# Kernel tuning notes

Measured on AMD Instinct MI355X. Metric: run time of the kernel, lower is better.

## Reference

```python
import jax, jax.numpy as jnp
import numpy as np

N, E, D = 100000, 1600000, 128
BN_EPS = 1e-5


def setup_inputs() -> dict:
    key = jax.random.key(0)
    k0, k1, k2 = jax.random.split(key, 3)
    x = jax.random.normal(k0, (N, D), dtype=jnp.float32)
    edge_index = jax.random.randint(k1, (2, E), 0, N, dtype=jnp.int32)
    # GCNConv weight (glorot-ish scale) and bias
    W = jax.random.normal(k2, (D, D), dtype=jnp.float32) * (1.0 / np.sqrt(D))
    b = jnp.zeros((D,), dtype=jnp.float32)
    # BatchNorm1d affine params
    gamma = jnp.ones((D,), dtype=jnp.float32)
    beta = jnp.zeros((D,), dtype=jnp.float32)
    # PReLU single shared slope (torch default init 0.25)
    a_prelu = jnp.asarray(0.25, dtype=jnp.float32)
    return {"x": x, "W": W, "b": b, "gamma": gamma, "beta": beta,
            "a_prelu": a_prelu, "edge_index": edge_index}


def reference(x, W, b, gamma, beta, a_prelu, edge_index):
    n = x.shape[0]
    loops = jnp.arange(n, dtype=edge_index.dtype)
    src = jnp.concatenate([edge_index[0], loops])  # [E+N]
    dst = jnp.concatenate([edge_index[1], loops])  # [E+N]

    # GCN symmetric normalization with self-loops: deg counts incoming edges
    deg = jax.ops.segment_sum(jnp.ones_like(dst, dtype=x.dtype), dst, num_segments=n)
    dinv = jax.lax.rsqrt(deg)  # deg >= 1 thanks to self-loops
    enorm = dinv[src] * dinv[dst]  # [E+N]

    xw = x @ W                                        # [N, D] transform first
    msg = xw[src] * enorm[:, None]                    # gather + scale
    out = jax.ops.segment_sum(msg, dst, num_segments=n) + b  # scatter-add

    # BatchNorm1d over nodes (training-mode batch statistics, biased var)
    mean = jnp.mean(out, axis=0)
    var = jnp.mean(jnp.square(out - mean), axis=0)
    out = (out - mean) * jax.lax.rsqrt(var + BN_EPS) * gamma + beta

    # PReLU (single shared slope); dropout is identity in eval mode
    out = jnp.where(out > 0, out, a_prelu * out)

    # identity residual (in_dim == out_dim)
    return out + x
```

## Files before the change

kernel.cpp:

```cpp
#include <hip/hip_runtime.h>

#define DIM 128
#define BSH 8
#define BUCK 256
#define CAP2 6144
#define BINCH 2048
#define MAXB 1024
#define FPT 12

typedef __attribute__((ext_vector_type(8))) short bf16x8;
typedef __attribute__((ext_vector_type(4))) float f32x4;
union U8 { uint4 u; bf16x8 b; };

static __device__ __forceinline__ unsigned f2bf_bits(float f) {
  unsigned u = __float_as_uint(f);
  return (u + 0x7fffu + ((u >> 16) & 1u)) >> 16;
}
static __device__ __forceinline__ unsigned packbf(float a, float b) {
  return (f2bf_bits(a) & 0xffffu) | (f2bf_bits(b) << 16);
}
static __device__ __forceinline__ float bfu_lo(unsigned pk) { return __uint_as_float(pk << 16); }
static __device__ __forceinline__ float bfu_hi(unsigned pk) { return __uint_as_float(pk & 0xffff0000u); }

static __device__ __forceinline__ int eread(const int* __restrict__ e, long long idx, int fl64) {
  return fl64 ? e[idx * 2] : e[idx];
}

__global__ __launch_bounds__(256) void k_prep(const int* __restrict__ eidx, int E,
                                              int* __restrict__ bcnt,
                                              unsigned* __restrict__ tmp2, int nbuck,
                                              const float* __restrict__ W,
                                              unsigned* __restrict__ wbt,
                                              int NBB) {
  __shared__ int hist[MAXB];
  __shared__ int lcur[MAXB];
  __shared__ int sfl;
  int bid = blockIdx.x;
  int tid = threadIdx.x;

  if (bid < NBB) {
    if (tid < 64) {
      int w = eidx[tid * 2 + 1];
      unsigned long long m = __ballot(w == 0);
      if (tid == 0) sfl = (__popcll(m) >= 48) ? 1 : 0;
    }
    for (int i = tid; i < nbuck; i += 256) hist[i] = 0;
    __syncthreads();
    int fl = sfl;
    long long ebase = (long long)bid * BINCH;
    unsigned pk[BINCH / 256];
    int bb[BINCH / 256];
#pragma unroll
    for (int it = 0; it < BINCH / 256; ++it) {
      long long e = ebase + it * 256 + tid;
      bb[it] = -1;
      if (e < E) {
        int s = eread(eidx, e, fl);
        int d = eread(eidx, (long long)E + e, fl);
        bb[it] = d >> BSH;
        pk[it] = ((unsigned)s << BSH) | (unsigned)(d & (BUCK - 1));
        atomicAdd(&hist[bb[it]], 1);
      }
    }
    __syncthreads();
    for (int b = tid; b < nbuck; b += 256) {
      int h = hist[b];
      lcur[b] = h ? atomicAdd(&bcnt[b], h) : 0;
    }
    __syncthreads();
#pragma unroll
    for (int it = 0; it < BINCH / 256; ++it) {
      if (bb[it] >= 0) {
        int sl = atomicAdd(&lcur[bb[it]], 1);
        if (sl < CAP2) tmp2[(unsigned)bb[it] * CAP2 + sl] = pk[it];
      }
    }
  } else {
    int w = (bid - NBB) * 256 + tid;
    int c = w >> 6, kk = w & 63;
    float lo = W[(unsigned)(2 * kk) * DIM + c];
    float hi = W[(unsigned)(2 * kk + 1) * DIM + c];
    wbt[(unsigned)c * 64 + kk] = packbf(lo, hi);
  }
}

__global__ __launch_bounds__(512) void k_histsort(const int* __restrict__ bcnt,
                                                  unsigned* __restrict__ tmp2,
                                                  int* __restrict__ ofs2,
                                                  int* __restrict__ deg,
                                                  const float* __restrict__ x,
                                                  unsigned* __restrict__ xb, int n) {
  __shared__ unsigned srt[CAP2];
  __shared__ int hist[BUCK];
  __shared__ int sc2[BUCK];
  __shared__ int lcur[BUCK];
  __shared__ float dls[BUCK];
  int b = blockIdx.x, tid = threadIdx.x;
  int cnt = bcnt[b];
  if (cnt > CAP2) cnt = CAP2;
  unsigned base = (unsigned)b * CAP2;
  if (tid < BUCK) hist[tid] = 0;
  __syncthreads();
  unsigned r[FPT];
#pragma unroll
  for (int u = 0; u < FPT; ++u) {
    int j = u * 512 + tid;
    r[u] = 0xffffffffu;
    if (j < cnt) {
      r[u] = tmp2[base + j];
      atomicAdd(&hist[r[u] & (BUCK - 1)], 1);
    }
  }
  __syncthreads();
  if (tid < 64) {
    int h0 = hist[tid * 4], h1 = hist[tid * 4 + 1];
    int h2 = hist[tid * 4 + 2], h3 = hist[tid * 4 + 3];
    int s = h0 + h1 + h2 + h3;
    int pre = s;
#pragma unroll
    for (int d = 1; d < 64; d <<= 1) {
      int t = __shfl_up(pre, d);
      if (tid >= d) pre += t;
    }
    pre -= s;
    int e0 = pre, e1 = pre + h0, e2 = e1 + h1, e3 = e2 + h2;
    sc2[tid * 4] = e0;     lcur[tid * 4] = e0;
    sc2[tid * 4 + 1] = e1; lcur[tid * 4 + 1] = e1;
    sc2[tid * 4 + 2] = e2; lcur[tid * 4 + 2] = e2;
    sc2[tid * 4 + 3] = e3; lcur[tid * 4 + 3] = e3;
  }
  __syncthreads();
#pragma unroll
  for (int u = 0; u < FPT; ++u) {
    if (r[u] != 0xffffffffu) {
      int sl = atomicAdd(&lcur[r[u] & (BUCK - 1)], 1);
      srt[sl] = r[u];
    }
  }
  if (tid < BUCK) dls[tid] = rsqrtf((float)(hist[tid] + 1));
  __syncthreads();
#pragma unroll
  for (int u = 0; u < FPT; ++u) {
    int j = u * 512 + tid;
    if (j < cnt) tmp2[base + j] = srt[j];
  }
  if (tid < BUCK) {
    int node = b * BUCK + tid;
    if (node < n) {
      ofs2[node] = (int)base + sc2[tid];
      deg[node] = hist[tid];
    }
  }
  int nb0 = b * BUCK;
#pragma unroll
  for (int it = 0; it < 32; ++it) {
    int idx = it * 512 + tid;
    int ln = idx >> 6, p = idx & 63;
    int node = nb0 + ln;
    if (node < n) {
      float di = dls[ln];
      float2 v = *(const float2*)(x + (size_t)node * DIM + p * 2);
      xb[(unsigned)node * 64 + p] = packbf(v.x * di, v.y * di);
    }
  }
}

__global__ __launch_bounds__(256) void k_agg(const unsigned* __restrict__ tmp2,
                                             const unsigned* __restrict__ xb,
                                             const int* __restrict__ ofs2,
                                             const int* __restrict__ deg,
                                             unsigned* __restrict__ agg, int n) {
  int wid = blockIdx.x * 4 + (threadIdx.x >> 6);
  int lane = threadIdx.x & 63;
  if (wid >= n) return;
  int dg = __builtin_amdgcn_readfirstlane(deg[wid]);
  float di = rsqrtf((float)(dg + 1));
  unsigned xp = xb[(unsigned)wid * 64 + lane];
  float ax = bfu_lo(xp), ay = bfu_hi(xp);
  int e = __builtin_amdgcn_readfirstlane(ofs2[wid]);
  int e1 = e + dg;
  for (; e + 16 <= e1; e += 16) {
    unsigned s[16];
#pragma unroll
    for (int u = 0; u < 16; ++u) s[u] = tmp2[(unsigned)(e + u)] >> BSH;
    unsigned v[16];
#pragma unroll
    for (int u = 0; u < 16; ++u) v[u] = xb[s[u] * 64 + lane];
#pragma unroll
    for (int u = 0; u < 16; ++u) { ax += bfu_lo(v[u]); ay += bfu_hi(v[u]); }
  }
  for (; e + 4 <= e1; e += 4) {
    unsigned s0 = tmp2[(unsigned)e] >> BSH, s1 = tmp2[(unsigned)e + 1] >> BSH;
    unsigned s2 = tmp2[(unsigned)e + 2] >> BSH, s3 = tmp2[(unsigned)e + 3] >> BSH;
    unsigned v0 = xb[s0 * 64 + lane], v1 = xb[s1 * 64 + lane];
    unsigned v2 = xb[s2 * 64 + lane], v3 = xb[s3 * 64 + lane];
    ax += bfu_lo(v0); ay += bfu_hi(v0);
    ax += bfu_lo(v1); ay += bfu_hi(v1);
    ax += bfu_lo(v2); ay += bfu_hi(v2);
    ax += bfu_lo(v3); ay += bfu_hi(v3);
  }
  for (; e < e1; ++e) {
    unsigned vv = xb[(tmp2[(unsigned)e] >> BSH) * 64 + lane];
    ax += bfu_lo(vv); ay += bfu_hi(vv);
  }
  agg[(unsigned)wid * 64 + lane] = packbf(ax * di, ay * di);
}

__global__ __launch_bounds__(256) void k_gemm(
    const unsigned* __restrict__ agg, const unsigned* __restrict__ wbt,
    const float* __restrict__ bias, unsigned* __restrict__ preb,
    float* __restrict__ part, int n) {
  __shared__ unsigned SM[64 * 68 + 128 * 68];
  unsigned* As2 = SM;
  unsigned* WsT = SM + 64 * 68;
  int tid = threadIdx.x;
  int base = blockIdx.x * 64;

#pragma unroll
  for (int it = 0; it < 32; ++it) {
    int idx = it * 256 + tid;
    int c = idx >> 6, kk = idx & 63;
    WsT[c * 68 + kk] = wbt[idx];
  }
#pragma unroll
  for (int it = 0; it < 16; ++it) {
    int idx = it * 256 + tid;
    int rl = idx >> 6, c2 = idx & 63;
    int g = base + rl; if (g >= n) g = n - 1;
    As2[rl * 68 + c2] = agg[(unsigned)g * 64 + c2];
  }
  __syncthreads();

  int w = tid >> 6, l = tid & 63;
  int lg = l >> 4, lr = l & 15;
  f32x4 acc[8];
#pragma unroll
  for (int nt = 0; nt < 8; ++nt) acc[nt] = (f32x4){0.f, 0.f, 0.f, 0.f};

#pragma unroll
  for (int kt = 0; kt < 4; ++kt) {
    U8 bfr;
    bfr.u = *(const uint4*)&As2[(w * 16 + lr) * 68 + kt * 16 + lg * 4];
#pragma unroll
    for (int nt = 0; nt < 8; ++nt) {
      U8 afr;
      afr.u = *(const uint4*)&WsT[(nt * 16 + lr) * 68 + kt * 16 + lg * 4];
      acc[nt] = __builtin_amdgcn_mfma_f32_16x16x32_bf16(afr.b, bfr.b, acc[nt], 0, 0, 0);
    }
  }
  __syncthreads();

  float* Cf = (float*)SM;
#pragma unroll
  for (int nt = 0; nt < 8; ++nt) {
    *(f32x4*)&Cf[(w * 16 + lr) * 132 + nt * 16 + lg * 4] = acc[nt];
  }
  __syncthreads();

  float* bn = Cf + 64 * 132;
  int c2 = tid & 63, g4 = tid >> 6;
  float b0 = bias[2 * c2], b1 = bias[2 * c2 + 1];
  float cs0 = 0.f, cs1 = 0.f, cq0 = 0.f, cq1 = 0.f;
#pragma unroll
  for (int it = 0; it < 16; ++it) {
    int m = it * 4 + g4;
    int gg = base + m;
    float2 vv = *(const float2*)&Cf[m * 132 + 2 * c2];
    float v0 = vv.x + b0, v1 = vv.y + b1;
    if (gg < n) {
      preb[(unsigned)gg * 64 + c2] = packbf(v0, v1);
      cs0 += v0; cq0 += v0 * v0;
      cs1 += v1; cq1 += v1 * v1;
    }
  }
  bn[g4 * 256 + 2 * c2] = cs0;
  bn[g4 * 256 + 2 * c2 + 1] = cs1;
  bn[g4 * 256 + 128 + 2 * c2] = cq0;
  bn[g4 * 256 + 128 + 2 * c2 + 1] = cq1;
  __syncthreads();
  part[(size_t)blockIdx.x * 256 + tid] = bn[tid] + bn[256 + tid] + bn[512 + tid] + bn[768 + tid];
}

__global__ __launch_bounds__(256) void k_redbn(const float* __restrict__ part, int nb,
                                               const float* __restrict__ gma,
                                               const float* __restrict__ bta,
                                               float* __restrict__ sc_,
                                               float* __restrict__ sh_, float invn) {
  __shared__ float r1[256], r2[256];
  int c = blockIdx.x, t = threadIdx.x;
  float s = 0.f, q = 0.f;
  for (int i = t; i < nb; i += 256) {
    s += part[(size_t)i * 256 + c];
    q += part[(size_t)i * 256 + 128 + c];
  }
  r1[t] = s; r2[t] = q;
  __syncthreads();
  for (int k = 128; k > 0; k >>= 1) {
    if (t < k) { r1[t] += r1[t + k]; r2[t] += r2[t + k]; }
    __syncthreads();
  }
  if (t == 0) {
    float mean = r1[0] * invn;
    float var = r2[0] * invn - mean * mean;
    float inv = rsqrtf(var + 1e-5f);
    float g = gma[c] * inv;
    sc_[c] = g;
    sh_[c] = bta[c] - mean * g;
  }
}

__global__ __launch_bounds__(256) void k_final(const unsigned* __restrict__ preb,
                                               const float* __restrict__ x,
                                               const float* __restrict__ sc,
                                               const float* __restrict__ sh,
                                               const float* __restrict__ apre,
                                               float* __restrict__ out, int n) {
  int t = blockIdx.x * 256 + threadIdx.x;
  int i = t >> 6, p = t & 63;
  if (i >= n) return;
  float a = apre[0];
  int c = p * 2;
  unsigned pk = preb[(unsigned)i * 64 + p];
  float t0 = bfu_lo(pk) * sc[c] + sh[c];
  float t1 = bfu_hi(pk) * sc[c + 1] + sh[c + 1];
  t0 = t0 > 0.f ? t0 : a * t0;
  t1 = t1 > 0.f ? t1 : a * t1;
  float2 xv = *(const float2*)(x + (size_t)i * DIM + c);
  t0 += xv.x;
  t1 += xv.y;
  *(float2*)(out + (size_t)i * DIM + c) = make_float2(t0, t1);
}

extern "C" void kernel_launch(void* const* d_in, const int* in_sizes, int n_in,
                              void* d_out, int out_size, void* d_ws, size_t ws_size,
                              hipStream_t stream) {
  (void)n_in; (void)out_size; (void)ws_size;
  const float* x    = (const float*)d_in[0];
  const float* W    = (const float*)d_in[1];
  const float* b    = (const float*)d_in[2];
  const float* gma  = (const float*)d_in[3];
  const float* bta  = (const float*)d_in[4];
  const float* apre = (const float*)d_in[5];
  const int* eidx   = (const int*)d_in[6];
  float* out        = (float*)d_out;

  const int N = in_sizes[0] / DIM;
  const int E = in_sizes[6] / 2;
  const int NB = (N + 63) / 64;
  const int NBUCK = (N + BUCK - 1) >> BSH;
  const int NBB = (E + BINCH - 1) / BINCH;
  const int NWT = 32;

  char* wsb = (char*)d_ws;
  size_t off_b = 0;
  auto take = [&](size_t bytes) -> void* {
    void* p = wsb + off_b;
    off_b += (bytes + 255) & ~(size_t)255;
    return p;
  };
  int*      bcnt  = (int*)     take((size_t)NBUCK * 4);
  int*      ofs2  = (int*)     take((size_t)N * 4);
  int*      deg   = (int*)     take((size_t)N * 4);
  unsigned* wbt   = (unsigned*)take((size_t)DIM * 64 * 4);
  unsigned* tmp2  = (unsigned*)take((size_t)NBUCK * CAP2 * 4);
  unsigned* xb    = (unsigned*)take((size_t)N * 64 * 4);
  unsigned* agg   = (unsigned*)take((size_t)N * 64 * 4);
  float*    part  = (float*)   take((size_t)NB * 256 * 4);
  float*    sc    = (float*)   take(DIM * 4);
  float*    sh    = (float*)   take(DIM * 4);
  unsigned* preb  = agg;

  hipMemsetAsync(bcnt, 0, (size_t)NBUCK * 4, stream);

  k_prep     <<<NBB + NWT, 256, 0, stream>>>(eidx, E, bcnt, tmp2, NBUCK, W, wbt, NBB);
  k_histsort <<<NBUCK, 512, 0, stream>>>(bcnt, tmp2, ofs2, deg, x, xb, N);
  k_agg      <<<(N + 3) / 4, 256, 0, stream>>>(tmp2, xb, ofs2, deg, agg, N);
  k_gemm     <<<NB, 256, 0, stream>>>(agg, wbt, b, preb, part, N);
  k_redbn    <<<DIM, 256, 0, stream>>>(part, NB, gma, bta, sc, sh, 1.0f / (float)N);
  k_final    <<<(N * 64 + 255) / 256, 256, 0, stream>>>(preb, x, sc, sh, apre, out, N);
}
```

Baseline: 271.8 us.

## Fuse neighbor aggregation into GEMM kernel with dynamic row scheduling in shared memory

Result: faster. 256.6 us (-5.6%).

```diff
diff --git a/kernel.cpp b/kernel.cpp
--- a/kernel.cpp
+++ b/kernel.cpp
@@ -153,107 +153,107 @@
   }
   int nb0 = b * BUCK;
 #pragma unroll
-  for (int it = 0; it < 32; ++it) {
+  for (int it = 0; it < 16; ++it) {
     int idx = it * 512 + tid;
-    int ln = idx >> 6, p = idx & 63;
+    int ln = idx >> 5, p = idx & 31;
     int node = nb0 + ln;
     if (node < n) {
       float di = dls[ln];
-      float2 v = *(const float2*)(x + (size_t)node * DIM + p * 2);
-      xb[(unsigned)node * 64 + p] = packbf(v.x * di, v.y * di);
-    }
-  }
-}
-
-__global__ __launch_bounds__(256) void k_agg(const unsigned* __restrict__ tmp2,
-                                             const unsigned* __restrict__ xb,
-                                             const int* __restrict__ ofs2,
-                                             const int* __restrict__ deg,
-                                             unsigned* __restrict__ agg, int n) {
-  int wid = blockIdx.x * 4 + (threadIdx.x >> 6);
-  int lane = threadIdx.x & 63;
-  if (wid >= n) return;
-  int dg = __builtin_amdgcn_readfirstlane(deg[wid]);
-  float di = rsqrtf((float)(dg + 1));
-  unsigned xp = xb[(unsigned)wid * 64 + lane];
-  float ax = bfu_lo(xp), ay = bfu_hi(xp);
-  int e = __builtin_amdgcn_readfirstlane(ofs2[wid]);
-  int e1 = e + dg;
-  for (; e + 16 <= e1; e += 16) {
-    unsigned s[16];
-#pragma unroll
-    for (int u = 0; u < 16; ++u) s[u] = tmp2[(unsigned)(e + u)] >> BSH;
-    unsigned v[16];
-#pragma unroll
-    for (int u = 0; u < 16; ++u) v[u] = xb[s[u] * 64 + lane];
-#pragma unroll
-    for (int u = 0; u < 16; ++u) { ax += bfu_lo(v[u]); ay += bfu_hi(v[u]); }
-  }
-  for (; e + 4 <= e1; e += 4) {
-    unsigned s0 = tmp2[(unsigned)e] >> BSH, s1 = tmp2[(unsigned)e + 1] >> BSH;
-    unsigned s2 = tmp2[(unsigned)e + 2] >> BSH, s3 = tmp2[(unsigned)e + 3] >> BSH;
-    unsigned v0 = xb[s0 * 64 + lane], v1 = xb[s1 * 64 + lane];
-    unsigned v2 = xb[s2 * 64 + lane], v3 = xb[s3 * 64 + lane];
-    ax += bfu_lo(v0); ay += bfu_hi(v0);
-    ax += bfu_lo(v1); ay += bfu_hi(v1);
-    ax += bfu_lo(v2); ay += bfu_hi(v2);
-    ax += bfu_lo(v3); ay += bfu_hi(v3);
-  }
-  for (; e < e1; ++e) {
-    unsigned vv = xb[(tmp2[(unsigned)e] >> BSH) * 64 + lane];
-    ax += bfu_lo(vv); ay += bfu_hi(vv);
-  }
-  agg[(unsigned)wid * 64 + lane] = packbf(ax * di, ay * di);
-}
-
-__global__ __launch_bounds__(256) void k_gemm(
-    const unsigned* __restrict__ agg, const unsigned* __restrict__ wbt,
-    const float* __restrict__ bias, unsigned* __restrict__ preb,
-    float* __restrict__ part, int n) {
+      float4 v = *(const float4*)(x + (size_t)node * DIM + p * 4);
+      uint2 o;
+      o.x = packbf(v.x * di, v.y * di);
+      o.y = packbf(v.z * di, v.w * di);
+      *(uint2*)&xb[(unsigned)node * 64 + p * 2] = o;
+    }
+  }
+}
+
+__global__ __launch_bounds__(1024) void k_agemm(
+    const unsigned* __restrict__ tmp2, const unsigned* __restrict__ xb,
+    const int* __restrict__ ofs2, const int* __restrict__ deg,
+    const unsigned* __restrict__ wbt, const float* __restrict__ bias,
+    unsigned* __restrict__ preb, float* __restrict__ part, int n) {
   __shared__ unsigned SM[64 * 68 + 128 * 68];
   unsigned* As2 = SM;
   unsigned* WsT = SM + 64 * 68;
+  __shared__ int nextn;
   int tid = threadIdx.x;
   int base = blockIdx.x * 64;
-
-#pragma unroll
-  for (int it = 0; it < 32; ++it) {
-    int idx = it * 256 + tid;
-    int c = idx >> 6, kk = idx & 63;
-    WsT[c * 68 + kk] = wbt[idx];
-  }
-#pragma unroll
-  for (int it = 0; it < 16; ++it) {
-    int idx = it * 256 + tid;
-    int rl = idx >> 6, c2 = idx & 63;
-    int g = base + rl; if (g >= n) g = n - 1;
-    As2[rl * 68 + c2] = agg[(unsigned)g * 64 + c2];
-  }
-  __syncthreads();
-
-  int w = tid >> 6, l = tid & 63;
-  int lg = l >> 4, lr = l & 15;
-  f32x4 acc[8];
-#pragma unroll
-  for (int nt = 0; nt < 8; ++nt) acc[nt] = (f32x4){0.f, 0.f, 0.f, 0.f};
-
+  int wv = tid >> 6, lane = tid & 63;
+
+#pragma unroll
+  for (int it = 0; it < 8; ++it) {
+    int idx = it * 1024 + tid;
+    WsT[(idx >> 6) * 68 + (idx & 63)] = wbt[idx];
+  }
+  if (tid == 0) nextn = 0;
+  __syncthreads();
+
+  for (;;) {
+    int rr = 0;
+    if (lane == 0) rr = atomicAdd(&nextn, 1);
+    rr = __shfl(rr, 0);
+    if (rr >= 64) break;
+    int node = base + rr;
+    float ax = 0.f, ay = 0.f, di = 1.f;
+    if (node < n) {
+      int dg = __builtin_amdgcn_readfirstlane(deg[node]);
+      int e = __builtin_amdgcn_readfirstlane(ofs2[node]);
+      di = rsqrtf((float)(dg + 1));
+      unsigned xp = xb[(unsigned)node * 64 + lane];
+      ax = bfu_lo(xp); ay = bfu_hi(xp);
+      int e1 = e + dg;
+      for (; e + 16 <= e1; e += 16) {
+        unsigned s[16];
+#pragma unroll
+        for (int u = 0; u < 16; ++u) s[u] = tmp2[(unsigned)(e + u)] >> BSH;
+        unsigned v[16];
+#pragma unroll
+        for (int u = 0; u < 16; ++u) v[u] = xb[s[u] * 64 + lane];
+#pragma unroll
+        for (int u = 0; u < 16; ++u) { ax += bfu_lo(v[u]); ay += bfu_hi(v[u]); }
+      }
+      for (; e + 4 <= e1; e += 4) {
+        unsigned s0 = tmp2[(unsigned)e] >> BSH, s1 = tmp2[(unsigned)e + 1] >> BSH;
+        unsigned s2 = tmp2[(unsigned)e + 2] >> BSH, s3 = tmp2[(unsigned)e + 3] >> BSH;
+        unsigned v0 = xb[s0 * 64 + lane], v1 = xb[s1 * 64 + lane];
+        unsigned v2 = xb[s2 * 64 + lane], v3 = xb[s3 * 64 + lane];
+        ax += bfu_lo(v0); ay += bfu_hi(v0);
+        ax += bfu_lo(v1); ay += bfu_hi(v1);
+        ax += bfu_lo(v2); ay += bfu_hi(v2);
+        ax += bfu_lo(v3); ay += bfu_hi(v3);
+      }
+      for (; e < e1; ++e) {
+        unsigned vv = xb[(tmp2[(unsigned)e] >> BSH) * 64 + lane];
+        ax += bfu_lo(vv); ay += bfu_hi(vv);
+      }
+    }
+    As2[rr * 68 + lane] = packbf(ax * di, ay * di);
+  }
+  __syncthreads();
+
+  int lg = lane >> 4, lr = lane & 15;
+  int rt = wv & 3, ctb = (wv >> 2) * 2;
+  f32x4 acc[2];
+  acc[0] = (f32x4){0.f, 0.f, 0.f, 0.f};
+  acc[1] = (f32x4){0.f, 0.f, 0.f, 0.f};
 #pragma unroll
   for (int kt = 0; kt < 4; ++kt) {
     U8 bfr;
-    bfr.u = *(const uint4*)&As2[(w * 16 + lr) * 68 + kt * 16 + lg * 4];
-#pragma unroll
-    for (int nt = 0; nt < 8; ++nt) {
+    bfr.u = *(const uint4*)&As2[(rt * 16 + lr) * 68 + kt * 16 + lg * 4];
+#pragma unroll
+    for (int t = 0; t < 2; ++t) {
       U8 afr;
-      afr.u = *(const uint4*)&WsT[(nt * 16 + lr) * 68 + kt * 16 + lg * 4];
-      acc[nt] = __builtin_amdgcn_mfma_f32_16x16x32_bf16(afr.b, bfr.b, acc[nt], 0, 0, 0);
+      afr.u = *(const uint4*)&WsT[((ctb + t) * 16 + lr) * 68 + kt * 16 + lg * 4];
+      acc[t] = __builtin_amdgcn_mfma_f32_16x16x32_bf16(afr.b, bfr.b, acc[t], 0, 0, 0);
     }
   }
   __syncthreads();
 
   float* Cf = (float*)SM;
 #pragma unroll
-  for (int nt = 0; nt < 8; ++nt) {
-    *(f32x4*)&Cf[(w * 16 + lr) * 132 + nt * 16 + lg * 4] = acc[nt];
+  for (int t = 0; t < 2; ++t) {
+    *(f32x4*)&Cf[(rt * 16 + lr) * 132 + (ctb + t) * 16 + lg * 4] = acc[t];
   }
   __syncthreads();
 
@@ -262,8 +262,8 @@
   float b0 = bias[2 * c2], b1 = bias[2 * c2 + 1];
   float cs0 = 0.f, cs1 = 0.f, cq0 = 0.f, cq1 = 0.f;
 #pragma unroll
-  for (int it = 0; it < 16; ++it) {
-    int m = it * 4 + g4;
+  for (int it = 0; it < 4; ++it) {
+    int m = it * 16 + g4;
     int gg = base + m;
     float2 vv = *(const float2*)&Cf[m * 132 + 2 * c2];
     float v0 = vv.x + b0, v1 = vv.y + b1;
@@ -278,7 +278,12 @@
   bn[g4 * 256 + 128 + 2 * c2] = cq0;
   bn[g4 * 256 + 128 + 2 * c2 + 1] = cq1;
   __syncthreads();
-  part[(size_t)blockIdx.x * 256 + tid] = bn[tid] + bn[256 + tid] + bn[512 + tid] + bn[768 + tid];
+  if (tid < 256) {
+    float v = 0.f;
+#pragma unroll
+    for (int g = 0; g < 16; ++g) v += bn[g * 256 + tid];
+    part[(size_t)blockIdx.x * 256 + tid] = v;
+  }
 }
 
 __global__ __launch_bounds__(256) void k_redbn(const float* __restrict__ part, int nb,
@@ -364,18 +369,16 @@
   unsigned* wbt   = (unsigned*)take((size_t)DIM * 64 * 4);
   unsigned* tmp2  = (unsigned*)take((size_t)NBUCK * CAP2 * 4);
   unsigned* xb    = (unsigned*)take((size_t)N * 64 * 4);
-  unsigned* agg   = (unsigned*)take((size_t)N * 64 * 4);
+  unsigned* preb  = (unsigned*)take((size_t)N * 64 * 4);
   float*    part  = (float*)   take((size_t)NB * 256 * 4);
   float*    sc    = (float*)   take(DIM * 4);
   float*    sh    = (float*)   take(DIM * 4);
-  unsigned* preb  = agg;
 
   hipMemsetAsync(bcnt, 0, (size_t)NBUCK * 4, stream);
 
   k_prep     <<<NBB + NWT, 256, 0, stream>>>(eidx, E, bcnt, tmp2, NBUCK, W, wbt, NBB);
   k_histsort <<<NBUCK, 512, 0, stream>>>(bcnt, tmp2, ofs2, deg, x, xb, N);
-  k_agg      <<<(N + 3) / 4, 256, 0, stream>>>(tmp2, xb, ofs2, deg, agg, N);
-  k_gemm     <<<NB, 256, 0, stream>>>(agg, wbt, b, preb, part, N);
+  k_agemm    <<<NB, 1024, 0, stream>>>(tmp2, xb, ofs2, deg, wbt, b, preb, part, N);
   k_redbn    <<<DIM, 256, 0, stream>>>(part, NB, gma, bta, sc, sh, 1.0f / (float)N);
   k_final    <<<(N * 64 + 255) / 256, 256, 0, stream>>>(preb, x, sc, sh, apre, out, N);
 }
```
